# Optimization experiments

Measured on AMD Instinct MI355X. Metric: run time of the kernel, lower is better.

The kernel has to match this reference:

```python
import jax, jax.numpy as jnp
import numpy as np

B, K, S, H, V, T = 32, 5, 64, 768, 30522, 40
SEP = 102


def setup_inputs() -> dict:
    key = jax.random.key(0)
    ks = jax.random.split(key, 8)
    s = 0.02
    return {
        "src": jax.random.normal(ks[0], (B, S, H), jnp.float32),
        "E": jax.random.normal(ks[1], (V, H), jnp.float32) * s,
        "Wa": jax.random.normal(ks[2], (H, H), jnp.float32) * s,
        "Ua": jax.random.normal(ks[3], (H, H), jnp.float32) * s,
        "va": jax.random.normal(ks[4], (H,), jnp.float32) * s,
        "W_ih": jax.random.normal(ks[5], (3 * H, 2 * H), jnp.float32) * s,
        "W_hh": jax.random.normal(ks[6], (3 * H, H), jnp.float32) * s,
        "b_ih": jnp.zeros((3 * H,), jnp.float32),
        "b_hh": jnp.zeros((3 * H,), jnp.float32),
        "Wo": jax.random.normal(ks[7], (V, H), jnp.float32) * s,
        "bo": jnp.zeros((V,), jnp.float32),
    }


def _decoder(tok, src, h, E, Wa, Ua, va, W_ih, W_hh, b_ih, b_hh, Wo, bo):
    # tok [N] int, src [N,S,H], h [N,H] -> (logits [N,V], h_new [N,H])
    emb = E[tok]                                              # [N,H]
    e = jnp.tanh(src @ Wa + (h @ Ua)[:, None, :]) @ va        # [N,S]
    a = jax.nn.softmax(e, axis=-1)
    ctx = jnp.einsum('ns,nsd->nd', a, src)                    # [N,H]
    x = jnp.concatenate([emb, ctx], axis=-1)                  # [N,2H]
    gx = x @ W_ih.T + b_ih
    gh = h @ W_hh.T + b_hh
    xr, xz, xn = jnp.split(gx, 3, axis=-1)
    hr, hz, hn = jnp.split(gh, 3, axis=-1)
    r = jax.nn.sigmoid(xr + hr)
    z = jax.nn.sigmoid(xz + hz)
    n = jnp.tanh(xn + r * hn)
    h2 = (1.0 - z) * n + z * h
    return h2 @ Wo.T + bo, h2


def _search(src, E, Wa, Ua, va, W_ih, W_hh, b_ih, b_hh, Wo, bo):
    P = (E, Wa, Ua, va, W_ih, W_hh, b_ih, b_hh, Wo, bo)
    # step 0: start token 102, zero hidden
    tok0 = jnp.full((B,), SEP, jnp.int32)
    logits, h = _decoder(tok0, src, jnp.zeros((B, H), src.dtype), *P)
    logp = jax.nn.log_softmax(logits, axis=-1)
    scores, toks = jax.lax.top_k(logp, K)                     # [B,K]
    hiddens = jnp.broadcast_to(h[:, None, :], (B, K, H))
    src_k = jnp.broadcast_to(src[:, None], (B, K, S, H)).reshape(B * K, S, H)
    no_prob = jnp.full((V,), -1e9, src.dtype).at[SEP].set(0.0)
    beam_mask = jnp.arange(K) < K - 1  # original normalizes only first k-1 segments

    def body(carry, _):
        toks, maps, hiddens, scores, ended, lengths = carry
        # parent hidden per beam (gather by backpointer), decode all beams at once
        h_in = jnp.take_along_axis(hiddens, maps[:, :, None], axis=1)  # [B,K,H]
        logits, h_new = _decoder(toks.reshape(-1), src_k, h_in.reshape(B * K, H), *P)
        logp = jax.nn.log_softmax(logits, axis=-1).reshape(B, K, V)
        logp = jnp.where(ended[:, :, None] == 0, logp, no_prob)
        lengths = lengths + (ended == 0).astype(lengths.dtype)
        cand = logp + scores[:, :, None]                      # [B,K,V]
        denom = jnp.where(beam_mask, lengths ** 0.7, 1.0)     # [B,K]
        norm = (cand / denom[:, :, None]).reshape(B, K * V)
        _, idx = jax.lax.top_k(norm, K)                       # [B,K]
        new_scores = jnp.take_along_axis(cand.reshape(B, K * V), idx, axis=1)
        new_toks = (idx % V).astype(jnp.int32)
        new_maps = (idx // V).astype(jnp.int32)
        ended = jnp.where(new_toks == SEP, 1.0, ended)
        new_carry = (new_toks, new_maps, h_new.reshape(B, K, H), new_scores, ended, lengths)
        return new_carry, (new_toks, new_maps)

    carry0 = (toks.astype(jnp.int32), jnp.zeros((B, K), jnp.int32), hiddens,
              scores, jnp.zeros((B, K), src.dtype), jnp.zeros((B, K), src.dtype))
    carryF, (toks_seq, maps_seq) = jax.lax.scan(body, carry0, None, length=T - 1)
    toks_all = jnp.concatenate([toks[None].astype(jnp.int32), toks_seq], axis=0)   # [T,B,K]
    maps_all = jnp.concatenate([jnp.zeros((1, B, K), jnp.int32), maps_seq], axis=0)
    final_scores = carryF[3]
    best = jnp.argmax(final_scores, axis=1).astype(jnp.int32)  # [B]

    def back(idx, tm):
        tk, mp = tm
        out = jnp.take_along_axis(tk, idx[:, None], axis=1)[:, 0]
        nxt = jnp.take_along_axis(mp, idx[:, None], axis=1)[:, 0]
        return nxt, out

    _, outs = jax.lax.scan(back, best, (toks_all, maps_all), reverse=True)
    return outs.T, final_scores  # tokens [B,T], scores [B,K]


def reference(src, E, Wa, Ua, va, W_ih, W_hh, b_ih, b_hh, Wo, bo):
    tokens, _ = _search(src, E, Wa, Ua, va, W_ih, W_hh, b_ih, b_hh, Wo, bo)
    return tokens
```

## Files before the change

### kernel.cpp

```cpp
#include <hip/hip_runtime.h>
#include <cmath>
#include <cfloat>

#define Hdim 768
#define Bb 32
#define Kb 5
#define Ss 64
#define Vv 30522
#define Tt 40
#define SEPTOK 102
#define PC 16

typedef __attribute__((ext_vector_type(2))) float  f32x2;
typedef __attribute__((ext_vector_type(4))) float  f32x4;

template<int CPT, bool PMAJOR>
__global__ __launch_bounds__(256) void gemmF_k(int P, int I, int xrs, int ld,
    const float* __restrict__ Xf, const float* __restrict__ W,
    const float* __restrict__ bias, float* __restrict__ out)
{
    __shared__ float xs[16][18];
    __shared__ float wt[CPT * 256][18];
    int tid = threadIdx.x;
    int n0 = blockIdx.y * 16;
    int i0 = blockIdx.x * (CPT * 256);
    float acc[CPT][16];
#pragma unroll
    for (int s = 0; s < CPT; s++)
#pragma unroll
        for (int r = 0; r < 16; r++) acc[s][r] = 0.f;

    int nch = P / PC;
    for (int c = 0; c < nch; c++) {
        int p0 = c * PC;
        __syncthreads();
        {
            int r = tid >> 4, p = tid & 15;
            xs[r][p] = Xf[(size_t)(n0 + r) * xrs + p0 + p];
        }
        if (PMAJOR) {
            const int LPR = CPT * 64;
            const int RPI = 256 / LPR;
            int i4 = (tid % LPR) * 4;
            int pl = tid / LPR;
#pragma unroll
            for (int it = 0; it < PC / RPI; ++it) {
                int p = pl + it * RPI;
                int gi = i0 + i4;
                f32x4 v = {0.f, 0.f, 0.f, 0.f};
                if (gi + 3 < I) {
                    v = *(const f32x4*)&W[(size_t)(p0 + p) * ld + gi];
                } else {
#pragma unroll
                    for (int q = 0; q < 4; q++)
                        if (gi + q < I) v[q] = W[(size_t)(p0 + p) * ld + gi + q];
                }
                wt[i4 + 0][p] = v[0]; wt[i4 + 1][p] = v[1];
                wt[i4 + 2][p] = v[2]; wt[i4 + 3][p] = v[3];
            }
        } else {
            int p4 = (tid & 3) * 4;
            int il = tid >> 2;
#pragma unroll
            for (int it = 0; it < CPT * 4; ++it) {
                int i_loc = il + it * 64;
                long long gi = i0 + i_loc;
                if (gi >= I) gi = I - 1;
                f32x4 v = *(const f32x4*)&W[(size_t)gi * ld + p0 + p4];
                wt[i_loc][p4 + 0] = v[0]; wt[i_loc][p4 + 1] = v[1];
                wt[i_loc][p4 + 2] = v[2]; wt[i_loc][p4 + 3] = v[3];
            }
        }
        __syncthreads();
        float part[CPT][16];
#pragma unroll
        for (int s = 0; s < CPT; s++)
#pragma unroll
            for (int r = 0; r < 16; r++) part[s][r] = 0.f;
#pragma unroll
        for (int p2 = 0; p2 < PC; p2 += 2) {
            f32x2 wv[CPT];
#pragma unroll
            for (int s = 0; s < CPT; s++)
                wv[s] = *(const f32x2*)&wt[s * 256 + tid][p2];
#pragma unroll
            for (int r = 0; r < 16; r++) {
                f32x2 xv = *(const f32x2*)&xs[r][p2];
#pragma unroll
                for (int s = 0; s < CPT; s++) {
                    part[s][r] = fmaf(xv.x, wv[s].x, part[s][r]);
                    part[s][r] = fmaf(xv.y, wv[s].y, part[s][r]);
                }
            }
        }
#pragma unroll
        for (int s = 0; s < CPT; s++)
#pragma unroll
            for (int r = 0; r < 16; r++) acc[s][r] = __fadd_rn(acc[s][r], part[s][r]);
    }
#pragma unroll
    for (int s = 0; s < CPT; s++) {
        int cs = i0 + s * 256 + tid;
        if (cs < I) {
            float bv = bias ? bias[cs] : 0.f;
#pragma unroll
            for (int r = 0; r < 16; r++) {
                float v = acc[s][r];
                if (bias) v = __fadd_rn(v, bv);
                out[(size_t)(n0 + r) * I + cs] = v;
            }
        }
    }
}

__global__ __launch_bounds__(256) void gather_k(int N, int Kcur,
    const int* __restrict__ maps, const int* __restrict__ toks,
    const float* __restrict__ h_beam, const float* __restrict__ E,
    float* __restrict__ h_g, float* __restrict__ xbuf)
{
    int n = blockIdx.x;
    if (n >= N) return;
    int b = n / Kcur;
    int tok = toks ? toks[n] : SEPTOK;
    const float* er = E + (size_t)tok * Hdim;
    if (maps) {
        const float* hs = h_beam + (size_t)(b * Kb + maps[n]) * Hdim;
        for (int j = threadIdx.x; j < Hdim; j += 256) {
            h_g[(size_t)n * Hdim + j]  = hs[j];
            xbuf[(size_t)n * 1536 + j] = er[j];
        }
    } else {
        for (int j = threadIdx.x; j < Hdim; j += 256) {
            h_g[(size_t)n * Hdim + j]  = 0.f;
            xbuf[(size_t)n * 1536 + j] = er[j];
        }
    }
}

__global__ __launch_bounds__(256) void bcast_k(const float* __restrict__ h_tmp,
                                               float* __restrict__ h_beam)
{
    int b = blockIdx.x;
    for (int j = threadIdx.x; j < Hdim; j += 256) {
        float v = h_tmp[(size_t)b * Hdim + j];
        for (int k = 0; k < Kb; k++)
            h_beam[(size_t)(b * Kb + k) * Hdim + j] = v;
    }
}

__global__ __launch_bounds__(256) void attn2_k(int N, int Kcur,
    const float* __restrict__ hUa, const float* __restrict__ srcWa,
    const float* __restrict__ src, const float* __restrict__ va,
    float* __restrict__ xbuf)
{
    __shared__ float hu[Hdim];
    __shared__ float va_s[Hdim];
    __shared__ float e_s[Ss];
    __shared__ float a_s[Ss];
    int n = blockIdx.x, tid = threadIdx.x;
    if (n >= N) return;
    int b = n / Kcur;
    for (int j = tid; j < Hdim; j += 256) {
        hu[j]   = hUa[(size_t)n * Hdim + j];
        va_s[j] = va[j];
    }
    __syncthreads();
    int wv = tid >> 6, ln = tid & 63;
    for (int s = wv * 16; s < wv * 16 + 16; s++) {
        const float* sw = srcWa + (size_t)(b * Ss + s) * Hdim;
        double p = 0.0;
        for (int j = ln; j < Hdim; j += 64) {
            float tv = (float)tanh((double)__fadd_rn(sw[j], hu[j]));
            p = ::fma((double)tv, (double)va_s[j], p);
        }
        for (int off = 32; off; off >>= 1) p += __shfl_down(p, off, 64);
        if (ln == 0) e_s[s] = (float)p;
    }
    __syncthreads();
    if (tid < 64) {
        float v = e_s[tid], m = v;
        for (int off = 32; off; off >>= 1) m = fmaxf(m, __shfl_xor(m, off, 64));
        float p = (float)exp((double)__fsub_rn(v, m));
        double sum = (double)p;
        for (int off = 32; off; off >>= 1) sum += __shfl_xor(sum, off, 64);
        a_s[tid] = __fdiv_rn(p, (float)sum);
    }
    __syncthreads();
    for (int j = tid; j < Hdim; j += 256) {
        double acc = 0.0;
        for (int s = 0; s < Ss; s++)
            acc = ::fma((double)a_s[s], (double)src[(size_t)(b * Ss + s) * Hdim + j], acc);
        xbuf[(size_t)n * 1536 + 768 + j] = (float)acc;
    }
}

__global__ __launch_bounds__(256) void gate_k(int N,
    const float* __restrict__ gx, const float* __restrict__ gh,
    const float* __restrict__ h_g, float* __restrict__ h_out)
{
    int idx = blockIdx.x * 256 + threadIdx.x;
    if (idx >= N * Hdim) return;
    int n = idx / Hdim, i = idx - n * Hdim;
    const float* gxr = gx + (size_t)n * 2304;
    const float* ghr = gh + (size_t)n * 2304;
    float xr = gxr[i], xz = gxr[768 + i], xn = gxr[1536 + i];
    float hr = ghr[i], hz = ghr[768 + i], hn = ghr[1536 + i];
    float r  = (float)(1.0 / (1.0 + exp(-(double)__fadd_rn(xr, hr))));
    float z  = (float)(1.0 / (1.0 + exp(-(double)__fadd_rn(xz, hz))));
    float nn = (float)tanh((double)__fadd_rn(xn, __fmul_rn(r, hn)));
    float hv = h_g[(size_t)n * Hdim + i];
    float h2 = __fadd_rn(__fmul_rn(__fsub_rn(1.f, z), nn), __fmul_rn(z, hv));
    h_out[(size_t)n * Hdim + i] = h2;
}

__global__ __launch_bounds__(256) void lse_k(int N,
    const float* __restrict__ logits, float* __restrict__ mx, float* __restrict__ lgs)
{
    __shared__ float  redf[256];
    __shared__ double redd[256];
    int n = blockIdx.x, tid = threadIdx.x;
    const float* lg = logits + (size_t)n * Vv;
    float m = -INFINITY;
    for (int v = tid; v < Vv; v += 256) m = fmaxf(m, lg[v]);
    redf[tid] = m; __syncthreads();
    for (int off = 128; off; off >>= 1) {
        if (tid < off) redf[tid] = fmaxf(redf[tid], redf[tid + off]);
        __syncthreads();
    }
    m = redf[0];
    double s = 0.0;
    for (int v = tid; v < Vv; v += 256) {
        float ex = (float)exp((double)__fsub_rn(lg[v], m));
        s += (double)ex;
    }
    redd[tid] = s; __syncthreads();
    for (int off = 128; off; off >>= 1) {
        if (tid < off) redd[tid] += redd[tid + off];
        __syncthreads();
    }
    if (tid == 0) {
        mx[n] = m;
        float sf = (float)redd[0];
        lgs[n] = (float)log((double)sf);
    }
}

__device__ __forceinline__ bool betterf(float va, int ja, float vb, int jb) {
    return (va > vb) || (va == vb && ja < jb);
}
__device__ __forceinline__ void ins5(float* tv, int* tj, float v, int j) {
    if (!betterf(v, j, tv[4], tj[4])) return;
    tv[4] = v; tj[4] = j;
#pragma unroll
    for (int q = 4; q > 0; q--) {
        if (betterf(tv[q], tj[q], tv[q - 1], tj[q - 1])) {
            float t = tv[q]; tv[q] = tv[q - 1]; tv[q - 1] = t;
            int  ti = tj[q]; tj[q] = tj[q - 1]; tj[q - 1] = ti;
        }
    }
}

__global__ __launch_bounds__(256) void topk5_k(int t,
    const float* __restrict__ logits, const float* __restrict__ mx, const float* __restrict__ lgs,
    float* scores, float* ended, float* lengths,
    int* toks_cur, int* maps_cur, int* toks_all, int* maps_all)
{
    __shared__ float sc_s[Kb], den_s[Kb], end_s[Kb], len_s[Kb], mx_s[Kb], lg_s[Kb];
    __shared__ float mv[256 * 5];
    __shared__ int   mj[256 * 5];
    __shared__ float rv[256];
    __shared__ int   rj[256];
    __shared__ int   selj[Kb];
    int b = blockIdx.x, tid = threadIdx.x;
    int Kcur = (t == 0) ? 1 : Kb;
    if (tid < Kb) {
        if (t == 0) {
            sc_s[tid] = 0.f; end_s[tid] = 0.f; len_s[tid] = 0.f; den_s[tid] = 1.f;
            mx_s[tid] = mx[b]; lg_s[tid] = lgs[b];
        } else {
            float e0 = ended[b * Kb + tid];
            float ln = __fadd_rn(lengths[b * Kb + tid], (e0 == 0.f) ? 1.f : 0.f);
            sc_s[tid]  = scores[b * Kb + tid];
            end_s[tid] = e0;
            len_s[tid] = ln;
            den_s[tid] = (tid < Kb - 1) ? (float)pow((double)ln, (double)0.7f) : 1.f;
            mx_s[tid]  = mx[b * Kb + tid];
            lg_s[tid]  = lgs[b * Kb + tid];
        }
    }
    __syncthreads();
    const float* lbase = logits + (size_t)b * Kcur * Vv;
    float tv[5]; int tj[5];
#pragma unroll
    for (int q = 0; q < 5; q++) { tv[q] = -INFINITY; tj[q] = 0x7fffffff; }
    for (int k = 0; k < Kcur; k++) {
        if (end_s[k] == 0.f) {
            float m = mx_s[k], l = lg_s[k], sck = sc_s[k], den = den_s[k];
            const float* lg = lbase + (size_t)k * Vv;
            for (int v = tid; v < Vv; v += 256) {
                float lp  = __fsub_rn(__fsub_rn(lg[v], m), l);
                float val = __fdiv_rn(__fadd_rn(lp, sck), den);
                ins5(tv, tj, val, k * Vv + v);
            }
        } else if (tid == 0) {
            float val = __fdiv_rn(sc_s[k], den_s[k]);
            ins5(tv, tj, val, k * Vv + SEPTOK);
        }
    }
#pragma unroll
    for (int q = 0; q < 5; q++) { mv[tid * 5 + q] = tv[q]; mj[tid * 5 + q] = tj[q]; }
    __syncthreads();
    for (int pass = 0; pass < Kb; pass++) {
        float bv = -INFINITY; int bj = 0x7fffffff;
#pragma unroll
        for (int q = 0; q < 5; q++) {
            float v = mv[tid * 5 + q]; int j = mj[tid * 5 + q];
            if (betterf(v, j, bv, bj)) { bv = v; bj = j; }
        }
        rv[tid] = bv; rj[tid] = bj;
        __syncthreads();
        for (int off = 128; off; off >>= 1) {
            if (tid < off) {
                float ov = rv[tid + off]; int oj = rj[tid + off];
                if (betterf(ov, oj, rv[tid], rj[tid])) { rv[tid] = ov; rj[tid] = oj; }
            }
            __syncthreads();
        }
        if (tid == 0) selj[pass] = rj[0];
        __syncthreads();
#pragma unroll
        for (int q = 0; q < 5; q++)
            if (mj[tid * 5 + q] == selj[pass]) { mv[tid * 5 + q] = -INFINITY; mj[tid * 5 + q] = 0x7fffffff; }
        __syncthreads();
    }
    if (tid == 0) {
        for (int q = 0; q < Kb; q++) {
            int jj = selj[q];
            int pk = jj / Vv, vv = jj - pk * Vv;
            float lp;
            if (end_s[pk] == 0.f)
                lp = __fsub_rn(__fsub_rn(lbase[(size_t)pk * Vv + vv], mx_s[pk]), lg_s[pk]);
            else
                lp = (vv == SEPTOK) ? 0.f : -1e9f;
            float cand = __fadd_rn(lp, sc_s[pk]);
            scores[b * Kb + q]   = cand;
            toks_cur[b * Kb + q] = vv;
            maps_cur[b * Kb + q] = (t == 0) ? 0 : pk;
            if (t == 0) {
                ended[b * Kb + q]   = 0.f;
                lengths[b * Kb + q] = 0.f;
            } else {
                ended[b * Kb + q]   = (vv == SEPTOK) ? 1.f : end_s[q];
                lengths[b * Kb + q] = len_s[q];
            }
            toks_all[(size_t)t * Bb * Kb + b * Kb + q] = vv;
            maps_all[(size_t)t * Bb * Kb + b * Kb + q] = (t == 0) ? 0 : pk;
        }
    }
}

__global__ void back_k(const float* __restrict__ scores,
                       const int* __restrict__ toks_all, const int* __restrict__ maps_all,
                       int* __restrict__ out)
{
    int b = threadIdx.x;
    if (b >= Bb) return;
    int best = 0; float bvv = scores[b * Kb];
    for (int k = 1; k < Kb; k++) {
        float v = scores[b * Kb + k];
        if (v > bvv) { bvv = v; best = k; }
    }
    int cur = best;
    for (int t = Tt - 1; t >= 0; t--) {
        out[b * Tt + t] = toks_all[t * Bb * Kb + b * Kb + cur];
        cur = maps_all[t * Bb * Kb + b * Kb + cur];
    }
}

extern "C" void kernel_launch(void* const* d_in, const int* in_sizes, int n_in,
                              void* d_out, int out_size, void* d_ws, size_t ws_size,
                              hipStream_t stream)
{
    const float* src  = (const float*)d_in[0];
    const float* E    = (const float*)d_in[1];
    const float* Wa   = (const float*)d_in[2];
    const float* Ua   = (const float*)d_in[3];
    const float* va   = (const float*)d_in[4];
    const float* W_ih = (const float*)d_in[5];
    const float* W_hh = (const float*)d_in[6];
    const float* b_ih = (const float*)d_in[7];
    const float* b_hh = (const float*)d_in[8];
    const float* Wo   = (const float*)d_in[9];
    const float* bo   = (const float*)d_in[10];
    int* out = (int*)d_out;

    char* w = (char*)d_ws;
    size_t used = 0;
    auto alloc = [&](size_t bytes) -> char* {
        char* p = w + used;
        used += (bytes + 255) & ~(size_t)255;
        return p;
    };
    float*  srcWa   = (float*) alloc((size_t)Bb * Ss * Hdim * 4);
    float*  h_beam  = (float*) alloc((size_t)Bb * Kb * Hdim * 4);
    float*  h_tmp   = (float*) alloc((size_t)Bb * Hdim * 4);
    float*  h_g     = (float*) alloc((size_t)Bb * Kb * Hdim * 4);
    float*  hUa     = (float*) alloc((size_t)Bb * Kb * Hdim * 4);
    float*  xbuf    = (float*) alloc((size_t)Bb * Kb * 1536 * 4);
    float*  gx      = (float*) alloc((size_t)Bb * Kb * 2304 * 4);
    float*  gh      = (float*) alloc((size_t)Bb * Kb * 2304 * 4);
    float*  logits  = (float*) alloc((size_t)Bb * Kb * Vv * 4);
    float*  mx      = (float*) alloc(Bb * Kb * 4);
    float*  lgs     = (float*) alloc(Bb * Kb * 4);
    float*  scores  = (float*) alloc(Bb * Kb * 4);
    float*  ended   = (float*) alloc(Bb * Kb * 4);
    float*  lengths = (float*) alloc(Bb * Kb * 4);
    int* toks_cur = (int*)alloc(Bb * Kb * 4);
    int* maps_cur = (int*)alloc(Bb * Kb * 4);
    int* toks_all = (int*)alloc((size_t)Tt * Bb * Kb * 4);
    int* maps_all = (int*)alloc((size_t)Tt * Bb * Kb * 4);

    gemmF_k<1, true><<<dim3(3, (Bb * Ss) / 16), 256, 0, stream>>>(
        Hdim, Hdim, Hdim, Hdim, src, Wa, nullptr, srcWa);

    for (int t = 0; t < Tt; t++) {
        int N  = (t == 0) ? Bb : Bb * Kb;
        int Kc = (t == 0) ? 1 : Kb;
        const int* mp = (t == 0) ? nullptr : maps_cur;
        const int* tk = (t == 0) ? nullptr : toks_cur;
        float* h_cur = (t == 0) ? h_tmp : h_beam;
        int nrt = N / 16;

        gather_k<<<N, 256, 0, stream>>>(N, Kc, mp, tk, h_beam, E, h_g, xbuf);
        gemmF_k<1, true><<<dim3(3, nrt), 256, 0, stream>>>(
            Hdim, Hdim, Hdim, Hdim, h_g, Ua, nullptr, hUa);
        attn2_k<<<N, 256, 0, stream>>>(N, Kc, hUa, srcWa, src, va, xbuf);
        gemmF_k<1, false><<<dim3(9, nrt), 256, 0, stream>>>(
            1536, 2304, 1536, 1536, xbuf, W_ih, b_ih, gx);
        gemmF_k<1, false><<<dim3(9, nrt), 256, 0, stream>>>(
            Hdim, 2304, Hdim, Hdim, h_g, W_hh, b_hh, gh);
        gate_k<<<(N * Hdim + 255) / 256, 256, 0, stream>>>(N, gx, gh, h_g, h_cur);
        if (t == 0)
            bcast_k<<<Bb, 256, 0, stream>>>(h_tmp, h_beam);
        gemmF_k<4, false><<<dim3(30, nrt), 256, 0, stream>>>(
            Hdim, Vv, Hdim, Hdim, h_cur, Wo, bo, logits);
        lse_k<<<N, 256, 0, stream>>>(N, logits, mx, lgs);
        topk5_k<<<Bb, 256, 0, stream>>>(t, logits, mx, lgs, scores, ended, lengths,
                                        toks_cur, maps_cur, toks_all, maps_all);
    }
    back_k<<<1, 64, 0, stream>>>(scores, toks_all, maps_all, out);
}
```

Measured before the change: 49.88 ms.

## Fuse whole beam-search loop into one cooperative persistent kernel with grid syncs

Replaces the ~400 per-step kernel launches with a single cooperative persistent kernel that loops over all decode steps and uses grid.sync between phases. Gathers of hidden state and embeddings move into the GEMM tile loader, and hidden state is ping-ponged between two buffers. GEMMs switch to a single 16-row, 256-column tile routine, with the Ua and W_hh products run in the same phase. This removes launch overhead and intermediate gather buffers, but adds many grid-wide barriers, a union shared-memory footprint that may lower occupancy, and a less register-blocked GEMM for the large vocabulary projection. The old multi-kernel path is kept as a fallback if the cooperative launch fails.

```diff
diff --git a/kernel.cpp b/kernel.cpp
--- a/kernel.cpp
+++ b/kernel.cpp
@@ -1,6 +1,8 @@
 #include <hip/hip_runtime.h>
+#include <hip/hip_cooperative_groups.h>
 #include <cmath>
-#include <cfloat>
+
+namespace cg = cooperative_groups;
 
 #define Hdim 768
 #define Bb 32
@@ -9,10 +11,391 @@
 #define Vv 30522
 #define Tt 40
 #define SEPTOK 102
-#define PC 16
-
-typedef __attribute__((ext_vector_type(2))) float  f32x2;
-typedef __attribute__((ext_vector_type(4))) float  f32x4;
+#define KCF 16
+#define PADWF 259
+
+typedef __attribute__((ext_vector_type(2))) float f32x2;
+typedef __attribute__((ext_vector_type(4))) float f32x4;
+
+struct Params {
+    const float *src, *E, *Wa, *Ua, *va, *W_ih, *W_hh, *b_ih, *b_hh, *Wo, *bo;
+    float *srcWa, *hA, *hB, *h_tmp, *h_gF, *hUa, *xbufF, *ctx, *gx, *gh, *logits;
+    float *mx, *lgs, *scores, *ended, *lengths;
+    int *toks_cur, *maps_cur, *toks_all, *maps_all, *outTok;
+};
+
+__device__ __forceinline__ bool betterf(float va, int ja, float vb, int jb) {
+    return (va > vb) || (va == vb && ja < jb);
+}
+__device__ __forceinline__ void ins5(float* tv, int* tj, float v, int j) {
+    if (!betterf(v, j, tv[4], tj[4])) return;
+    tv[4] = v; tj[4] = j;
+#pragma unroll
+    for (int q = 4; q > 0; q--) {
+        if (betterf(tv[q], tj[q], tv[q - 1], tj[q - 1])) {
+            float t = tv[q]; tv[q] = tv[q - 1]; tv[q - 1] = t;
+            int  ti = tj[q]; tj[q] = tj[q - 1]; tj[q - 1] = ti;
+        }
+    }
+}
+
+union SMemF {
+    struct { float xs[16][20]; float wtp[KCF][PADWF]; } g;
+    struct { float hu[Hdim]; float va_s[Hdim]; float e_s[Ss]; float a_s[Ss]; } at;
+    struct { float redf[256]; double redd[256]; } ls;
+    struct {
+        float sc[Kb], den[Kb], end[Kb], len[Kb], mxs[Kb], lgv[Kb];
+        float mv[256 * 5]; int mj[256 * 5];
+        float rv[256]; int rj[256]; int selj[Kb];
+    } tk;
+};
+
+__device__ void gemm_tile16(SMemF& sm, const Params& P, int t, int xsrc,
+    int n0, int i0, int Pdim, const float* __restrict__ W, int ldW, bool imaj,
+    const float* __restrict__ bias, float* __restrict__ outp, int ldO, int Icap)
+{
+    int tid = threadIdx.x;
+    const float* h_old = (t & 1) ? P.hB : P.hA;
+    const float* h_new = (t & 1) ? P.hA : P.hB;
+    int rowMul = (t == 0) ? Kb : 1;
+    float acc[16];
+#pragma unroll
+    for (int r = 0; r < 16; r++) acc[r] = 0.f;
+
+    for (int c0 = 0; c0 < Pdim; c0 += KCF) {
+        __syncthreads();
+        {
+            int r = tid >> 4, p = tid & 15;
+            int n = n0 + r;
+            float v = 0.f;
+            if (xsrc == 0) {
+                if (t != 0) {
+                    int bk = (n / Kb) * Kb + P.maps_cur[n];
+                    v = h_old[(size_t)bk * Hdim + c0 + p];
+                }
+            } else if (xsrc == 1) {
+                int pg = c0 + p;
+                if (pg < Hdim) {
+                    int tok = (t == 0) ? SEPTOK : P.toks_cur[n];
+                    v = P.E[(size_t)tok * Hdim + pg];
+                } else {
+                    v = P.ctx[(size_t)n * Hdim + (pg - Hdim)];
+                }
+            } else if (xsrc == 2) {
+                v = h_new[((size_t)n * rowMul) * Hdim + c0 + p];
+            } else {
+                v = P.src[(size_t)n * Hdim + c0 + p];
+            }
+            sm.g.xs[r][p] = v;
+        }
+        if (imaj) {
+            int gi = i0 + tid; if (gi >= Icap) gi = Icap - 1;
+            const float* wp = W + (size_t)gi * ldW + c0;
+#pragma unroll
+            for (int p4 = 0; p4 < 4; p4++) {
+                f32x4 a = *(const f32x4*)(wp + p4 * 4);
+#pragma unroll
+                for (int u = 0; u < 4; u++) sm.g.wtp[p4 * 4 + u][tid] = a[u];
+            }
+        } else {
+            int p = tid & 15, cl = (tid >> 4) * 16;
+            const float* wp = W + (size_t)(c0 + p) * ldW + i0 + cl;
+#pragma unroll
+            for (int e = 0; e < 4; e++) {
+                f32x4 a = *(const f32x4*)(wp + e * 4);
+#pragma unroll
+                for (int u = 0; u < 4; u++) sm.g.wtp[p][cl + e * 4 + u] = a[u];
+            }
+        }
+        __syncthreads();
+        float part[16];
+#pragma unroll
+        for (int r = 0; r < 16; r++) part[r] = 0.f;
+#pragma unroll
+        for (int p4 = 0; p4 < KCF / 4; p4++) {
+            float w0 = sm.g.wtp[p4 * 4 + 0][tid];
+            float w1 = sm.g.wtp[p4 * 4 + 1][tid];
+            float w2 = sm.g.wtp[p4 * 4 + 2][tid];
+            float w3 = sm.g.wtp[p4 * 4 + 3][tid];
+#pragma unroll
+            for (int r = 0; r < 16; r++) {
+                f32x4 xv = *(const f32x4*)&sm.g.xs[r][p4 * 4];
+                float s = part[r];
+                s = fmaf(xv.x, w0, s);
+                s = fmaf(xv.y, w1, s);
+                s = fmaf(xv.z, w2, s);
+                s = fmaf(xv.w, w3, s);
+                part[r] = s;
+            }
+        }
+#pragma unroll
+        for (int r = 0; r < 16; r++) acc[r] = __fadd_rn(acc[r], part[r]);
+    }
+    int ic = i0 + tid;
+    if (ic < Icap) {
+        float bv = bias ? bias[ic] : 0.f;
+#pragma unroll
+        for (int r = 0; r < 16; r++) {
+            float v = acc[r];
+            if (bias) v = __fadd_rn(v, bv);
+            outp[(size_t)(n0 + r) * ldO + ic] = v;
+        }
+    }
+}
+
+__global__ __launch_bounds__(256) void srcwa_k(Params P)
+{
+    __shared__ SMemF sm;
+    int rt = blockIdx.x / 3, ct = blockIdx.x % 3;
+    gemm_tile16(sm, P, 1, 3, rt * 16, ct * 256, Hdim, P.Wa, Hdim, false, nullptr,
+                P.srcWa, Hdim, Hdim);
+}
+
+__global__ __launch_bounds__(256) void fused_k(Params P)
+{
+    cg::grid_group grid = cg::this_grid();
+    __shared__ SMemF sm;
+    const int blk = blockIdx.x, tid = threadIdx.x;
+    const int gdim = gridDim.x;
+
+    for (int t = 0; t < Tt; t++) {
+        int N = (t == 0) ? Bb : Bb * Kb;
+        int Kcur = (t == 0) ? 1 : Kb;
+        int nrt = N / 16;
+        float* h_new = (t & 1) ? P.hA : P.hB;
+        const float* h_old = (t & 1) ? P.hB : P.hA;
+
+        {
+            int nUa = nrt * 3, nHH = nrt * 9;
+            for (int task = blk; task < nUa + nHH; task += gdim) {
+                if (task < nUa) {
+                    int rt = task / 3, ct = task % 3;
+                    gemm_tile16(sm, P, t, 0, rt * 16, ct * 256, Hdim,
+                                P.Ua, Hdim, false, nullptr, P.hUa, Hdim, Hdim);
+                } else {
+                    int k = task - nUa; int rt = k / 9, ct = k % 9;
+                    gemm_tile16(sm, P, t, 0, rt * 16, ct * 256, Hdim,
+                                P.W_hh, Hdim, true, P.b_hh, P.gh, 2304, 2304);
+                }
+            }
+        }
+        grid.sync();
+
+        for (int n = blk; n < N; n += gdim) {
+            int b = n / Kcur;
+            for (int j = tid; j < Hdim; j += 256) {
+                sm.at.hu[j]   = P.hUa[(size_t)n * Hdim + j];
+                sm.at.va_s[j] = P.va[j];
+            }
+            __syncthreads();
+            int wv = tid >> 6, ln = tid & 63;
+            for (int s = wv * 16; s < wv * 16 + 16; s++) {
+                const float* sw = P.srcWa + (size_t)(b * Ss + s) * Hdim;
+                double p = 0.0;
+                for (int j = ln; j < Hdim; j += 64) {
+                    float tv = (float)tanh((double)__fadd_rn(sw[j], sm.at.hu[j]));
+                    p = ::fma((double)tv, (double)sm.at.va_s[j], p);
+                }
+                for (int off = 32; off; off >>= 1) p += __shfl_down(p, off, 64);
+                if (ln == 0) sm.at.e_s[s] = (float)p;
+            }
+            __syncthreads();
+            if (tid < 64) {
+                float v = sm.at.e_s[tid], m = v;
+                for (int off = 32; off; off >>= 1) m = fmaxf(m, __shfl_xor(m, off, 64));
+                float p = (float)exp((double)__fsub_rn(v, m));
+                double sum = (double)p;
+                for (int off = 32; off; off >>= 1) sum += __shfl_xor(sum, off, 64);
+                sm.at.a_s[tid] = __fdiv_rn(p, (float)sum);
+            }
+            __syncthreads();
+            for (int j = tid; j < Hdim; j += 256) {
+                double acc = 0.0;
+                for (int s = 0; s < Ss; s++)
+                    acc = ::fma((double)sm.at.a_s[s],
+                                (double)P.src[(size_t)(b * Ss + s) * Hdim + j], acc);
+                P.ctx[(size_t)n * Hdim + j] = (float)acc;
+            }
+            __syncthreads();
+        }
+        grid.sync();
+
+        for (int task = blk; task < nrt * 9; task += gdim) {
+            int rt = task / 9, ct = task % 9;
+            gemm_tile16(sm, P, t, 1, rt * 16, ct * 256, 1536,
+                        P.W_ih, 1536, true, P.b_ih, P.gx, 2304, 2304);
+        }
+        grid.sync();
+
+        for (int idx = blk * 256 + tid; idx < N * Hdim; idx += gdim * 256) {
+            int n = idx / Hdim, i = idx - n * Hdim;
+            const float* gxr = P.gx + (size_t)n * 2304;
+            const float* ghr = P.gh + (size_t)n * 2304;
+            float xr = gxr[i], xz = gxr[768 + i], xn = gxr[1536 + i];
+            float hr = ghr[i], hz = ghr[768 + i], hn = ghr[1536 + i];
+            float r  = (float)(1.0 / (1.0 + exp(-(double)__fadd_rn(xr, hr))));
+            float z  = (float)(1.0 / (1.0 + exp(-(double)__fadd_rn(xz, hz))));
+            float nn = (float)tanh((double)__fadd_rn(xn, __fmul_rn(r, hn)));
+            float hv = (t == 0) ? 0.f
+                     : h_old[((size_t)((n / Kb) * Kb + P.maps_cur[n])) * Hdim + i];
+            float h2 = __fadd_rn(__fmul_rn(__fsub_rn(1.f, z), nn), __fmul_rn(z, hv));
+            if (t == 0) {
+                for (int k = 0; k < Kb; k++)
+                    h_new[(size_t)(n * Kb + k) * Hdim + i] = h2;
+            } else {
+                h_new[(size_t)n * Hdim + i] = h2;
+            }
+        }
+        grid.sync();
+
+        for (int task = blk; task < nrt * 120; task += gdim) {
+            int rt = task / 120, ct = task % 120;
+            gemm_tile16(sm, P, t, 2, rt * 16, ct * 256, Hdim,
+                        P.Wo, Hdim, true, P.bo, P.logits, Vv, Vv);
+        }
+        grid.sync();
+
+        for (int n = blk; n < N; n += gdim) {
+            const float* lg = P.logits + (size_t)n * Vv;
+            float m = -INFINITY;
+            for (int v = tid; v < Vv; v += 256) m = fmaxf(m, lg[v]);
+            sm.ls.redf[tid] = m; __syncthreads();
+            for (int off = 128; off; off >>= 1) {
+                if (tid < off) sm.ls.redf[tid] = fmaxf(sm.ls.redf[tid], sm.ls.redf[tid + off]);
+                __syncthreads();
+            }
+            m = sm.ls.redf[0];
+            double s = 0.0;
+            for (int v = tid; v < Vv; v += 256) {
+                float ex = (float)exp((double)__fsub_rn(lg[v], m));
+                s += (double)ex;
+            }
+            __syncthreads();
+            sm.ls.redd[tid] = s; __syncthreads();
+            for (int off = 128; off; off >>= 1) {
+                if (tid < off) sm.ls.redd[tid] += sm.ls.redd[tid + off];
+                __syncthreads();
+            }
+            if (tid == 0) {
+                P.mx[n] = m;
+                float sf = (float)sm.ls.redd[0];
+                P.lgs[n] = (float)log((double)sf);
+            }
+            __syncthreads();
+        }
+        grid.sync();
+
+        for (int b = blk; b < Bb; b += gdim) {
+            if (tid < Kb) {
+                if (t == 0) {
+                    sm.tk.sc[tid] = 0.f; sm.tk.end[tid] = 0.f; sm.tk.len[tid] = 0.f;
+                    sm.tk.den[tid] = 1.f;
+                    sm.tk.mxs[tid] = P.mx[b]; sm.tk.lgv[tid] = P.lgs[b];
+                } else {
+                    float e0 = P.ended[b * Kb + tid];
+                    float ln = __fadd_rn(P.lengths[b * Kb + tid], (e0 == 0.f) ? 1.f : 0.f);
+                    sm.tk.sc[tid]  = P.scores[b * Kb + tid];
+                    sm.tk.end[tid] = e0;
+                    sm.tk.len[tid] = ln;
+                    sm.tk.den[tid] = (tid < Kb - 1) ? (float)pow((double)ln, (double)0.7f) : 1.f;
+                    sm.tk.mxs[tid] = P.mx[b * Kb + tid];
+                    sm.tk.lgv[tid] = P.lgs[b * Kb + tid];
+                }
+            }
+            __syncthreads();
+            const float* lbase = P.logits + (size_t)b * Kcur * Vv;
+            float tv[5]; int tj[5];
+#pragma unroll
+            for (int q = 0; q < 5; q++) { tv[q] = -INFINITY; tj[q] = 0x7fffffff; }
+            for (int k = 0; k < Kcur; k++) {
+                if (sm.tk.end[k] == 0.f) {
+                    float m = sm.tk.mxs[k], l = sm.tk.lgv[k];
+                    float sck = sm.tk.sc[k], den = sm.tk.den[k];
+                    const float* lg = lbase + (size_t)k * Vv;
+                    for (int v = tid; v < Vv; v += 256) {
+                        float lp  = __fsub_rn(__fsub_rn(lg[v], m), l);
+                        float val = __fdiv_rn(__fadd_rn(lp, sck), den);
+                        ins5(tv, tj, val, k * Vv + v);
+                    }
+                } else if (tid == 0) {
+                    float val = __fdiv_rn(sm.tk.sc[k], sm.tk.den[k]);
+                    ins5(tv, tj, val, k * Vv + SEPTOK);
+                }
+            }
+#pragma unroll
+            for (int q = 0; q < 5; q++) { sm.tk.mv[tid * 5 + q] = tv[q]; sm.tk.mj[tid * 5 + q] = tj[q]; }
+            __syncthreads();
+            for (int pass = 0; pass < Kb; pass++) {
+                float bv = -INFINITY; int bj = 0x7fffffff;
+#pragma unroll
+                for (int q = 0; q < 5; q++) {
+                    float v = sm.tk.mv[tid * 5 + q]; int j = sm.tk.mj[tid * 5 + q];
+                    if (betterf(v, j, bv, bj)) { bv = v; bj = j; }
+                }
+                sm.tk.rv[tid] = bv; sm.tk.rj[tid] = bj;
+                __syncthreads();
+                for (int off = 128; off; off >>= 1) {
+                    if (tid < off) {
+                        float ov = sm.tk.rv[tid + off]; int oj = sm.tk.rj[tid + off];
+                        if (betterf(ov, oj, sm.tk.rv[tid], sm.tk.rj[tid])) {
+                            sm.tk.rv[tid] = ov; sm.tk.rj[tid] = oj;
+                        }
+                    }
+                    __syncthreads();
+                }
+                if (tid == 0) sm.tk.selj[pass] = sm.tk.rj[0];
+                __syncthreads();
+#pragma unroll
+                for (int q = 0; q < 5; q++)
+                    if (sm.tk.mj[tid * 5 + q] == sm.tk.selj[pass]) {
+                        sm.tk.mv[tid * 5 + q] = -INFINITY; sm.tk.mj[tid * 5 + q] = 0x7fffffff;
+                    }
+                __syncthreads();
+            }
+            if (tid == 0) {
+                for (int q = 0; q < Kb; q++) {
+                    int jj = sm.tk.selj[q];
+                    int pk = jj / Vv, vv = jj - pk * Vv;
+                    float lp;
+                    if (sm.tk.end[pk] == 0.f)
+                        lp = __fsub_rn(__fsub_rn(lbase[(size_t)pk * Vv + vv], sm.tk.mxs[pk]),
+                                       sm.tk.lgv[pk]);
+                    else
+                        lp = (vv == SEPTOK) ? 0.f : -1e9f;
+                    float cand = __fadd_rn(lp, sm.tk.sc[pk]);
+                    P.scores[b * Kb + q]   = cand;
+                    P.toks_cur[b * Kb + q] = vv;
+                    P.maps_cur[b * Kb + q] = (t == 0) ? 0 : pk;
+                    if (t == 0) {
+                        P.ended[b * Kb + q]   = 0.f;
+                        P.lengths[b * Kb + q] = 0.f;
+                    } else {
+                        P.ended[b * Kb + q]   = (vv == SEPTOK) ? 1.f : sm.tk.end[q];
+                        P.lengths[b * Kb + q] = sm.tk.len[q];
+                    }
+                    P.toks_all[(size_t)t * Bb * Kb + b * Kb + q] = vv;
+                    P.maps_all[(size_t)t * Bb * Kb + b * Kb + q] = (t == 0) ? 0 : pk;
+                }
+            }
+            __syncthreads();
+        }
+        grid.sync();
+    }
+
+    if (blk == 0 && tid < Bb) {
+        int b = tid;
+        int best = 0; float bvv = P.scores[b * Kb];
+        for (int k = 1; k < Kb; k++) {
+            float v = P.scores[b * Kb + k];
+            if (v > bvv) { bvv = v; best = k; }
+        }
+        int cur = best;
+        for (int t = Tt - 1; t >= 0; t--) {
+            P.outTok[b * Tt + t] = P.toks_all[t * Bb * Kb + b * Kb + cur];
+            cur = P.maps_all[t * Bb * Kb + b * Kb + cur];
+        }
+    }
+}
 
 template<int CPT, bool PMAJOR>
 __global__ __launch_bounds__(256) void gemmF_k(int P, int I, int xrs, int ld,
@@ -30,9 +413,9 @@
 #pragma unroll
         for (int r = 0; r < 16; r++) acc[s][r] = 0.f;
 
-    int nch = P / PC;
+    int nch = P / 16;
     for (int c = 0; c < nch; c++) {
-        int p0 = c * PC;
+        int p0 = c * 16;
         __syncthreads();
         {
             int r = tid >> 4, p = tid & 15;
@@ -44,7 +427,7 @@
             int i4 = (tid % LPR) * 4;
             int pl = tid / LPR;
 #pragma unroll
-            for (int it = 0; it < PC / RPI; ++it) {
+            for (int it = 0; it < 16 / RPI; ++it) {
                 int p = pl + it * RPI;
                 int gi = i0 + i4;
                 f32x4 v = {0.f, 0.f, 0.f, 0.f};
@@ -78,7 +461,7 @@
 #pragma unroll
             for (int r = 0; r < 16; r++) part[s][r] = 0.f;
 #pragma unroll
-        for (int p2 = 0; p2 < PC; p2 += 2) {
+        for (int p2 = 0; p2 < 16; p2 += 2) {
             f32x2 wv[CPT];
 #pragma unroll
             for (int s = 0; s < CPT; s++)
@@ -242,21 +625,6 @@
         mx[n] = m;
         float sf = (float)redd[0];
         lgs[n] = (float)log((double)sf);
-    }
-}
-
-__device__ __forceinline__ bool betterf(float va, int ja, float vb, int jb) {
-    return (va > vb) || (va == vb && ja < jb);
-}
-__device__ __forceinline__ void ins5(float* tv, int* tj, float v, int j) {
-    if (!betterf(v, j, tv[4], tj[4])) return;
-    tv[4] = v; tj[4] = j;
-#pragma unroll
-    for (int q = 4; q > 0; q--) {
-        if (betterf(tv[q], tj[q], tv[q - 1], tj[q - 1])) {
-            float t = tv[q]; tv[q] = tv[q - 1]; tv[q - 1] = t;
-            int  ti = tj[q]; tj[q] = tj[q - 1]; tj[q - 1] = ti;
-        }
     }
 }
 
@@ -381,18 +749,19 @@
                               void* d_out, int out_size, void* d_ws, size_t ws_size,
                               hipStream_t stream)
 {
-    const float* src  = (const float*)d_in[0];
-    const float* E    = (const float*)d_in[1];
-    const float* Wa   = (const float*)d_in[2];
-    const float* Ua   = (const float*)d_in[3];
-    const float* va   = (const float*)d_in[4];
-    const float* W_ih = (const float*)d_in[5];
-    const float* W_hh = (const float*)d_in[6];
-    const float* b_ih = (const float*)d_in[7];
-    const float* b_hh = (const float*)d_in[8];
-    const float* Wo   = (const float*)d_in[9];
-    const float* bo   = (const float*)d_in[10];
-    int* out = (int*)d_out;
+    Params P;
+    P.src  = (const float*)d_in[0];
+    P.E    = (const float*)d_in[1];
+    P.Wa   = (const float*)d_in[2];
+    P.Ua   = (const float*)d_in[3];
+    P.va   = (const float*)d_in[4];
+    P.W_ih = (const float*)d_in[5];
+    P.W_hh = (const float*)d_in[6];
+    P.b_ih = (const float*)d_in[7];
+    P.b_hh = (const float*)d_in[8];
+    P.Wo   = (const float*)d_in[9];
+    P.bo   = (const float*)d_in[10];
+    P.outTok = (int*)d_out;
 
     char* w = (char*)d_ws;
     size_t used = 0;
@@ -401,52 +770,74 @@
         used += (bytes + 255) & ~(size_t)255;
         return p;
     };
-    float*  srcWa   = (float*) alloc((size_t)Bb * Ss * Hdim * 4);
-    float*  h_beam  = (float*) alloc((size_t)Bb * Kb * Hdim * 4);
-    float*  h_tmp   = (float*) alloc((size_t)Bb * Hdim * 4);
-    float*  h_g     = (float*) alloc((size_t)Bb * Kb * Hdim * 4);
-    float*  hUa     = (float*) alloc((size_t)Bb * Kb * Hdim * 4);
-    float*  xbuf    = (float*) alloc((size_t)Bb * Kb * 1536 * 4);
-    float*  gx      = (float*) alloc((size_t)Bb * Kb * 2304 * 4);
-    float*  gh      = (float*) alloc((size_t)Bb * Kb * 2304 * 4);
-    float*  logits  = (float*) alloc((size_t)Bb * Kb * Vv * 4);
-    float*  mx      = (float*) alloc(Bb * Kb * 4);
-    float*  lgs     = (float*) alloc(Bb * Kb * 4);
-    float*  scores  = (float*) alloc(Bb * Kb * 4);
-    float*  ended   = (float*) alloc(Bb * Kb * 4);
-    float*  lengths = (float*) alloc(Bb * Kb * 4);
-    int* toks_cur = (int*)alloc(Bb * Kb * 4);
-    int* maps_cur = (int*)alloc(Bb * Kb * 4);
-    int* toks_all = (int*)alloc((size_t)Tt * Bb * Kb * 4);
-    int* maps_all = (int*)alloc((size_t)Tt * Bb * Kb * 4);
-
-    gemmF_k<1, true><<<dim3(3, (Bb * Ss) / 16), 256, 0, stream>>>(
-        Hdim, Hdim, Hdim, Hdim, src, Wa, nullptr, srcWa);
-
-    for (int t = 0; t < Tt; t++) {
-        int N  = (t == 0) ? Bb : Bb * Kb;
-        int Kc = (t == 0) ? 1 : Kb;
-        const int* mp = (t == 0) ? nullptr : maps_cur;
-        const int* tk = (t == 0) ? nullptr : toks_cur;
-        float* h_cur = (t == 0) ? h_tmp : h_beam;
-        int nrt = N / 16;
-
-        gather_k<<<N, 256, 0, stream>>>(N, Kc, mp, tk, h_beam, E, h_g, xbuf);
-        gemmF_k<1, true><<<dim3(3, nrt), 256, 0, stream>>>(
-            Hdim, Hdim, Hdim, Hdim, h_g, Ua, nullptr, hUa);
-        attn2_k<<<N, 256, 0, stream>>>(N, Kc, hUa, srcWa, src, va, xbuf);
-        gemmF_k<1, false><<<dim3(9, nrt), 256, 0, stream>>>(
-            1536, 2304, 1536, 1536, xbuf, W_ih, b_ih, gx);
-        gemmF_k<1, false><<<dim3(9, nrt), 256, 0, stream>>>(
-            Hdim, 2304, Hdim, Hdim, h_g, W_hh, b_hh, gh);
-        gate_k<<<(N * Hdim + 255) / 256, 256, 0, stream>>>(N, gx, gh, h_g, h_cur);
-        if (t == 0)
-            bcast_k<<<Bb, 256, 0, stream>>>(h_tmp, h_beam);
-        gemmF_k<4, false><<<dim3(30, nrt), 256, 0, stream>>>(
-            Hdim, Vv, Hdim, Hdim, h_cur, Wo, bo, logits);
-        lse_k<<<N, 256, 0, stream>>>(N, logits, mx, lgs);
-        topk5_k<<<Bb, 256, 0, stream>>>(t, logits, mx, lgs, scores, ended, lengths,
-                                        toks_cur, maps_cur, toks_all, maps_all);
-    }
-    back_k<<<1, 64, 0, stream>>>(scores, toks_all, maps_all, out);
-}
+    P.srcWa   = (float*)alloc((size_t)Bb * Ss * Hdim * 4);
+    P.hA      = (float*)alloc((size_t)Bb * Kb * Hdim * 4);
+    P.hB      = (float*)alloc((size_t)Bb * Kb * Hdim * 4);
+    P.h_tmp   = (float*)alloc((size_t)Bb * Hdim * 4);
+    P.h_gF    = (float*)alloc((size_t)Bb * Kb * Hdim * 4);
+    P.hUa     = (float*)alloc((size_t)Bb * Kb * Hdim * 4);
+    P.xbufF   = (float*)alloc((size_t)Bb * Kb * 1536 * 4);
+    P.ctx     = (float*)alloc((size_t)Bb * Kb * Hdim * 4);
+    P.gx      = (float*)alloc((size_t)Bb * Kb * 2304 * 4);
+    P.gh      = (float*)alloc((size_t)Bb * Kb * 2304 * 4);
+    P.logits  = (float*)alloc((size_t)Bb * Kb * Vv * 4);
+    P.mx      = (float*)alloc(Bb * Kb * 4);
+    P.lgs     = (float*)alloc(Bb * Kb * 4);
+    P.scores  = (float*)alloc(Bb * Kb * 4);
+    P.ended   = (float*)alloc(Bb * Kb * 4);
+    P.lengths = (float*)alloc(Bb * Kb * 4);
+    P.toks_cur = (int*)alloc(Bb * Kb * 4);
+    P.maps_cur = (int*)alloc(Bb * Kb * 4);
+    P.toks_all = (int*)alloc((size_t)Tt * Bb * Kb * 4);
+    P.maps_all = (int*)alloc((size_t)Tt * Bb * Kb * 4);
+
+    srcwa_k<<<dim3(128 * 3), 256, 0, stream>>>(P);
+
+    int dev = 0;
+    (void)hipGetDevice(&dev);
+    int nCU = 256;
+    (void)hipDeviceGetAttribute(&nCU, hipDeviceAttributeMultiprocessorCount, dev);
+    int maxAct = 0;
+    if (hipOccupancyMaxActiveBlocksPerMultiprocessor(&maxAct, fused_k, 256, 0)
+            != hipSuccess || maxAct < 1)
+        maxAct = 1;
+    long long gridLL = (long long)maxAct * (long long)nCU;
+    if (gridLL > 2048) gridLL = 2048;
+    if (gridLL < 1) gridLL = 1;
+    dim3 grid((unsigned)gridLL);
+
+    void* args[] = { (void*)&P };
+    hipError_t err = hipLaunchCooperativeKernel((void*)fused_k, grid, dim3(256),
+                                                args, 0, stream);
+    if (err != hipSuccess) {
+        (void)hipGetLastError();
+        for (int t = 0; t < Tt; t++) {
+            int N  = (t == 0) ? Bb : Bb * Kb;
+            int Kc = (t == 0) ? 1 : Kb;
+            const int* mp = (t == 0) ? nullptr : P.maps_cur;
+            const int* tk = (t == 0) ? nullptr : P.toks_cur;
+            float* h_beam = P.hA;
+            float* h_cur = (t == 0) ? P.h_tmp : h_beam;
+            int nrt = N / 16;
+
+            gather_k<<<N, 256, 0, stream>>>(N, Kc, mp, tk, h_beam, P.E, P.h_gF, P.xbufF);
+            gemmF_k<1, true><<<dim3(3, nrt), 256, 0, stream>>>(
+                Hdim, Hdim, Hdim, Hdim, P.h_gF, P.Ua, nullptr, P.hUa);
+            attn2_k<<<N, 256, 0, stream>>>(N, Kc, P.hUa, P.srcWa, P.src, P.va, P.xbufF);
+            gemmF_k<1, false><<<dim3(9, nrt), 256, 0, stream>>>(
+                1536, 2304, 1536, 1536, P.xbufF, P.W_ih, P.b_ih, P.gx);
+            gemmF_k<1, false><<<dim3(9, nrt), 256, 0, stream>>>(
+                Hdim, 2304, Hdim, Hdim, P.h_gF, P.W_hh, P.b_hh, P.gh);
+            gate_k<<<(N * Hdim + 255) / 256, 256, 0, stream>>>(N, P.gx, P.gh, P.h_gF, h_cur);
+            if (t == 0)
+                bcast_k<<<Bb, 256, 0, stream>>>(P.h_tmp, h_beam);
+            gemmF_k<4, false><<<dim3(30, nrt), 256, 0, stream>>>(
+                Hdim, Vv, Hdim, Hdim, h_cur, P.Wo, P.bo, P.logits);
+            lse_k<<<N, 256, 0, stream>>>(N, P.logits, P.mx, P.lgs);
+            topk5_k<<<Bb, 256, 0, stream>>>(t, P.logits, P.mx, P.lgs, P.scores,
+                                            P.ended, P.lengths, P.toks_cur, P.maps_cur,
+                                            P.toks_all, P.maps_all);
+        }
+        back_k<<<1, 64, 0, stream>>>(P.scores, P.toks_all, P.maps_all, P.outTok);
+    }
+}
```

Result: slower. 56.71 ms (+13.7%).
